# Optimization experiments

Measured on AMD Instinct MI355X. Metric: run time of the kernel, lower is better.

## Reference

```python
import jax, jax.numpy as jnp
import numpy as np

# Architecture constants pinned by the source script
D_MODEL = 2      # input_size / problemDim
ED = 64          # d_inner = expand_factor * d_model = hidden_size
N = 32           # d_state
K = 16           # d_conv
DT_RANK = 1      # ceil(d_model / 16)
NC = 4           # num_classes
B, L = 16, 2048


def setup_inputs() -> dict:
    key = jax.random.key(0)
    ks = jax.random.split(key, 16)
    rn = lambda k, shape, sc=0.1: jax.random.normal(k, shape, jnp.float32) * sc
    return {
        "x": jax.random.normal(ks[0], (B, L, D_MODEL), jnp.float32),
        "norm_w": jnp.ones((D_MODEL,), jnp.float32),
        "w_in": rn(ks[1], (D_MODEL, 2 * ED)),            # in_proj (no bias)
        "conv_w": rn(ks[2], (ED, 1, K)),                  # depthwise causal conv
        "conv_b": rn(ks[3], (ED,)),
        "w_xproj": rn(ks[4], (ED, DT_RANK + 2 * N)),      # x_proj (no bias)
        "w_dt": rn(ks[5], (DT_RANK, ED)),                 # dt_proj
        "b_dt": rn(ks[6], (ED,)),
        "A_log": jnp.log(jnp.tile(jnp.arange(1, N + 1, dtype=jnp.float32), (ED, 1))),
        "D_skip": jnp.ones((ED,), jnp.float32),
        "w_out": rn(ks[7], (ED, ED)),                     # out_proj (classifier mode: d_inner->d_inner)
        "b_out": rn(ks[8], (ED,)),
        "w_fc": rn(ks[9], (ED, ED)),
        "b_fc": rn(ks[10], (ED,)),
        "w_cls": rn(ks[11], (ED, NC)),
        "b_cls": rn(ks[12], (NC,)),
        "w_reg": rn(ks[13], (ED, 1)),
        "b_reg": rn(ks[14], (1,)),
    }


def _rmsnorm(x, w, eps=1e-5):
    return x * jax.lax.rsqrt(jnp.mean(x * x, axis=-1, keepdims=True) + eps) * w


def _silu(x):
    return x * jax.nn.sigmoid(x)


def reference(x, norm_w, w_in, conv_w, conv_b, w_xproj, w_dt, b_dt, A_log, D_skip,
              w_out, b_out, w_fc, b_fc, w_cls, b_cls, w_reg, b_reg):
    # --- Mamba block (n_layers = 1, classifier mode: no residual back to d_model) ---
    h = _rmsnorm(x, norm_w)                                # [B,L,D]
    xz = h @ w_in                                          # [B,L,2*ED]
    xb, z = jnp.split(xz, 2, axis=-1)
    # depthwise causal conv over time (torch pads K-1 both sides then slices [:L] == left-pad K-1)
    xc = jnp.transpose(xb, (0, 2, 1))                      # [B,ED,L]
    xc = jax.lax.conv_general_dilated(
        xc, conv_w, window_strides=(1,), padding=[(K - 1, 0)],
        feature_group_count=ED, dimension_numbers=("NCH", "OIH", "NCH"))
    xc = xc + conv_b[None, :, None]
    xb = _silu(jnp.transpose(xc, (0, 2, 1)))               # [B,L,ED]
    # input-dependent SSM parameters
    dbc = xb @ w_xproj                                     # [B,L,dt_rank+2N]
    delta = jax.nn.softplus(dbc[..., :DT_RANK] @ w_dt + b_dt)   # [B,L,ED]
    Bm = dbc[..., DT_RANK:DT_RANK + N]                     # [B,L,N]
    C = dbc[..., DT_RANK + N:]                             # [B,L,N]
    A = -jnp.exp(A_log)                                    # [ED,N]
    dA = jnp.exp(delta[..., None] * A)                     # [B,L,ED,N]
    dBx = delta[..., None] * Bm[:, :, None, :] * xb[..., None]  # [B,L,ED,N]

    # selective scan: h_t = dA_t * h_{t-1} + dBx_t ; y_t = <h_t, C_t>
    def step(hst, inp):
        dA_t, dBx_t, C_t = inp
        hst = dA_t * hst + dBx_t                           # [B,ED,N]
        y = jnp.einsum("ben,bn->be", hst, C_t)
        return hst, y

    h0 = jnp.zeros((x.shape[0], ED, N), x.dtype)
    xs = (jnp.transpose(dA, (1, 0, 2, 3)),
          jnp.transpose(dBx, (1, 0, 2, 3)),
          jnp.transpose(C, (1, 0, 2)))
    _, ys = jax.lax.scan(step, h0, xs)                     # [L,B,ED]
    y = jnp.transpose(ys, (1, 0, 2)) + D_skip * xb         # [B,L,ED]
    y = y * _silu(z)                                       # gate
    out = y @ w_out + b_out                                # [B,L,ED]

    last = out[:, -1, :]                                   # [B,ED]
    hs = jax.nn.relu(last @ w_fc + b_fc)
    class_logits = hs @ w_cls + b_cls                      # [B,NC]
    mass_pred = (hs @ w_reg + b_reg)[:, 0]                 # [B]
    return class_logits, mass_pred
```

## Files before the change

kernel.cpp:

```cpp
#include <hip/hip_runtime.h>
#include <math.h>

#define BB 16
#define LL 2048
#define ED 64
#define NN 32
#define KK 16
#define NCHUNK 64
#define CH 32
#define NBLK (BB * NCHUNK)
#define NSEG 4
#define CPS (NCHUNK / NSEG)
#define XS (ED + 4)

__global__ __launch_bounds__(256) void k1_featscan(
    const float* __restrict__ x, const float* __restrict__ norm_w,
    const float* __restrict__ w_in, const float* __restrict__ conv_w,
    const float* __restrict__ conv_b, const float* __restrict__ w_xproj,
    const float* __restrict__ w_dt, const float* __restrict__ b_dt,
    float* __restrict__ sbuf, float* __restrict__ dsumbuf,
    float* __restrict__ xlast, float* __restrict__ zl, float* __restrict__ cl)
{
    const int bx = blockIdx.x;
    const int b = bx >> 6, ti = bx & 63;
    const int l0 = ti * CH;
    const int tid = threadIdx.x;

    __shared__ __align__(16) float xbl[CH][XS];
    __shared__ float hh[2 * (CH + KK - 1)];
    __shared__ __align__(16) float wdt[ED];
    __shared__ __align__(16) float wxs[ED][NN];
    __shared__ float dsp[4][ED];
    __shared__ __align__(16) union U {
        float pre[CH + KK - 1][ED];
        struct {
            float2 dlrl[CH][ED];
            float bml[CH][36];
            float dtr[CH];
        } sb;
    } u;

    for (int idx = tid; idx < ED * NN; idx += 256) {
        int e = idx >> 5, j = idx & 31;
        wxs[e][j] = w_xproj[e * 65 + 1 + j];
    }
    if (tid < ED) wdt[tid] = w_xproj[tid * 65];

    if (tid < 2 * (CH + KK - 1)) {
        int p = tid >> 1, c = tid & 1;
        int l = l0 - (KK - 1) + p;
        hh[tid] = (l >= 0) ? x[(b * LL + l) * 2 + c] : 0.f;
    }
    __syncthreads();
    if (tid < CH + KK - 1) {
        float x0 = hh[2 * tid], x1 = hh[2 * tid + 1];
        float s = rsqrtf(0.5f * (x0 * x0 + x1 * x1) + 1e-5f);
        hh[2 * tid]     = x0 * s * norm_w[0];
        hh[2 * tid + 1] = x1 * s * norm_w[1];
    }
    __syncthreads();
    {
        const int e = tid & 63;
        const float w0 = w_in[e], w1 = w_in[128 + e];
        for (int idx = tid; idx < (CH + KK - 1) * ED; idx += 256) {
            int p = idx >> 6;
            u.pre[p][e] = hh[2 * p] * w0 + hh[2 * p + 1] * w1;
        }
    }
    __syncthreads();
    {
        const int e = tid & 63, tg = tid >> 6, t0 = tg * 8;
        const float4 c0 = *(const float4*)(conv_w + e * KK);
        const float4 c1 = *(const float4*)(conv_w + e * KK + 4);
        const float4 c2 = *(const float4*)(conv_w + e * KK + 8);
        const float4 c3 = *(const float4*)(conv_w + e * KK + 12);
        const float cw[KK] = {c0.x, c0.y, c0.z, c0.w, c1.x, c1.y, c1.z, c1.w,
                              c2.x, c2.y, c2.z, c2.w, c3.x, c3.y, c3.z, c3.w};
        float w[8 + KK - 1];
        #pragma unroll
        for (int i = 0; i < 8 + KK - 1; ++i) w[i] = u.pre[t0 + i][e];
        const float bias = conv_b[e];
        #pragma unroll
        for (int i = 0; i < 8; ++i) {
            float acc = bias;
            #pragma unroll
            for (int k = 0; k < KK; ++k) acc = __fmaf_rn(cw[k], w[i + k], acc);
            xbl[t0 + i][e] = acc / (1.f + __expf(-acc));
        }
    }
    __syncthreads();
    {
        const int t = tid & 31, jg = tid >> 5;
        float a0 = 0.f, a1 = 0.f, a2 = 0.f, a3 = 0.f;
        for (int e = 0; e < ED; e += 4) {
            const float4 xv = *(const float4*)&xbl[t][e];
            const float4 w0 = *(const float4*)&wxs[e + 0][jg * 4];
            const float4 w1 = *(const float4*)&wxs[e + 1][jg * 4];
            const float4 w2 = *(const float4*)&wxs[e + 2][jg * 4];
            const float4 w3 = *(const float4*)&wxs[e + 3][jg * 4];
            a0 = __fmaf_rn(xv.x, w0.x, a0); a1 = __fmaf_rn(xv.x, w0.y, a1);
            a2 = __fmaf_rn(xv.x, w0.z, a2); a3 = __fmaf_rn(xv.x, w0.w, a3);
            a0 = __fmaf_rn(xv.y, w1.x, a0); a1 = __fmaf_rn(xv.y, w1.y, a1);
            a2 = __fmaf_rn(xv.y, w1.z, a2); a3 = __fmaf_rn(xv.y, w1.w, a3);
            a0 = __fmaf_rn(xv.z, w2.x, a0); a1 = __fmaf_rn(xv.z, w2.y, a1);
            a2 = __fmaf_rn(xv.z, w2.z, a2); a3 = __fmaf_rn(xv.z, w2.w, a3);
            a0 = __fmaf_rn(xv.w, w3.x, a0); a1 = __fmaf_rn(xv.w, w3.y, a1);
            a2 = __fmaf_rn(xv.w, w3.z, a2); a3 = __fmaf_rn(xv.w, w3.w, a3);
        }
        u.sb.bml[t][jg * 4 + 0] = a0;
        u.sb.bml[t][jg * 4 + 1] = a1;
        u.sb.bml[t][jg * 4 + 2] = a2;
        u.sb.bml[t][jg * 4 + 3] = a3;
    }
    if (tid < CH) {
        float acc = 0.f;
        for (int e = 0; e < ED; e += 4) {
            const float4 xv = *(const float4*)&xbl[tid][e];
            const float4 wv = *(const float4*)&wdt[e];
            acc = __fmaf_rn(xv.x, wv.x, acc);
            acc = __fmaf_rn(xv.y, wv.y, acc);
            acc = __fmaf_rn(xv.z, wv.z, acc);
            acc = __fmaf_rn(xv.w, wv.w, acc);
        }
        u.sb.dtr[tid] = acc;
    }
    if (ti == NCHUNK - 1) {
        if (tid < NN) {
            float acc = 0.f;
            for (int e = 0; e < ED; ++e)
                acc = __fmaf_rn(xbl[CH - 1][e], w_xproj[e * 65 + 33 + tid], acc);
            cl[b * NN + tid] = acc;
        } else if (tid >= 64 && tid < 128) {
            int e = tid - 64;
            int pl = 2 * (CH + KK - 2);
            zl[b * ED + e] = hh[pl] * w_in[64 + e] + hh[pl + 1] * w_in[192 + e];
        } else if (tid >= 128 && tid < 192) {
            int e = tid - 128;
            xlast[b * ED + e] = xbl[CH - 1][e];
        }
    }
    __syncthreads();
    {
        const int e = tid & 63, tg = tid >> 6;
        const float wde = w_dt[e], bde = b_dt[e];
        float dpart = 0.f;
        #pragma unroll
        for (int k = 0; k < 8; ++k) {
            int s = tg + 4 * k;
            float v = __fmaf_rn(u.sb.dtr[s], wde, bde);
            float d = (v > 15.f) ? v : __logf(1.f + __expf(v));
            dpart += d;
            u.sb.dlrl[s][e] = make_float2(__expf(-d), d * xbl[s][e]);
        }
        dsp[tg][e] = dpart;
    }
    __syncthreads();
    {
        const int e = tid & 63, ng = tid >> 6, n0 = ng * 8;
        float S[8];
        #pragma unroll
        for (int j = 0; j < 8; ++j) S[j] = 0.f;

        for (int s = 0; s < CH; ++s) {
            const float2 rd = u.sb.dlrl[s][e];
            const float r = rd.x, dx = rd.y;
            const float4 b0 = *(const float4*)&u.sb.bml[s][n0];
            const float4 b1 = *(const float4*)&u.sb.bml[s][n0 + 4];
            float r2 = r * r, r4 = r2 * r2, r8 = r4 * r4;
            float bb1 = (ng & 1) ? r8 : 1.f;
            float bb2 = (ng & 2) ? r8 * r8 : 1.f;
            float m = r * bb1 * bb2;
            S[0] = __fmaf_rn(m, S[0], dx * b0.x); m *= r;
            S[1] = __fmaf_rn(m, S[1], dx * b0.y); m *= r;
            S[2] = __fmaf_rn(m, S[2], dx * b0.z); m *= r;
            S[3] = __fmaf_rn(m, S[3], dx * b0.w); m *= r;
            S[4] = __fmaf_rn(m, S[4], dx * b1.x); m *= r;
            S[5] = __fmaf_rn(m, S[5], dx * b1.y); m *= r;
            S[6] = __fmaf_rn(m, S[6], dx * b1.z); m *= r;
            S[7] = __fmaf_rn(m, S[7], dx * b1.w);
        }

        const int gbase = (ti * BB + b) * (ED * NN) + e * NN + n0;
        *(float4*)&sbuf[gbase]     = make_float4(S[0], S[1], S[2], S[3]);
        *(float4*)&sbuf[gbase + 4] = make_float4(S[4], S[5], S[6], S[7]);
        if (tid < 64) {
            float Dsum = dsp[0][tid] + dsp[1][tid] + dsp[2][tid] + dsp[3][tid];
            dsumbuf[(ti * BB + b) * ED + tid] = Dsum;
        }
    }
}

__global__ __launch_bounds__(256) void k2_fold(
    const float* __restrict__ sbuf, const float* __restrict__ dsumbuf,
    const float* __restrict__ A_log, float* __restrict__ hfin)
{
    const int tid = threadIdx.x;
    const int sid = tid & 63, seg = tid >> 6;
    const int state = blockIdx.x * 64 + sid;
    const int b = state >> 11, r = state & 2047;
    const int e = r >> 5, n = r & 31;
    const float A = -__expf(A_log[e * NN + n]);

    float M = 1.f, S = 0.f;
    const int c0 = seg * CPS;
    #pragma unroll
    for (int k = 0; k < CPS; ++k) {
        const int c = c0 + k;
        float m = __expf(A * dsumbuf[(c * BB + b) * ED + e]);
        S = __fmaf_rn(m, S, sbuf[(c * BB + b) * (ED * NN) + r]);
        M *= m;
    }

    __shared__ float Ms[NSEG][64], Ss[NSEG][64];
    Ms[seg][sid] = M;
    Ss[seg][sid] = S;
    __syncthreads();
    if (seg == 0) {
        float h = S;
        #pragma unroll
        for (int k = 1; k < NSEG; ++k)
            h = __fmaf_rn(Ms[k][sid], h, Ss[k][sid]);
        hfin[state] = h;
    }
}

__global__ __launch_bounds__(256) void k3_tail(
    const float* __restrict__ hfin, const float* __restrict__ cl,
    const float* __restrict__ zl, const float* __restrict__ xlast,
    const float* __restrict__ D_skip, const float* __restrict__ w_out,
    const float* __restrict__ b_out, const float* __restrict__ w_fc,
    const float* __restrict__ b_fc, const float* __restrict__ w_cls,
    const float* __restrict__ b_cls, const float* __restrict__ w_reg,
    const float* __restrict__ b_reg, float* __restrict__ out)
{
    const int b = blockIdx.x, tid = threadIdx.x;
    const int e = tid & 63, ng = tid >> 6, n0 = ng * 8;

    __shared__ float part[4][ED];
    __shared__ float ylds[ED], olds[ED], hlds[ED];

    float acc;
    {
        const float4 h0 = *(const float4*)&hfin[b * (ED * NN) + e * NN + n0];
        const float4 h1 = *(const float4*)&hfin[b * (ED * NN) + e * NN + n0 + 4];
        const float4 q0 = *(const float4*)&cl[b * NN + n0];
        const float4 q1 = *(const float4*)&cl[b * NN + n0 + 4];
        acc = h0.x * q0.x + h0.y * q0.y + h0.z * q0.z + h0.w * q0.w
            + h1.x * q1.x + h1.y * q1.y + h1.z * q1.z + h1.w * q1.w;
    }
    part[ng][e] = acc;
    __syncthreads();

    if (tid < ED) {
        float y = part[0][tid] + part[1][tid] + part[2][tid] + part[3][tid];
        y = __fmaf_rn(D_skip[tid], xlast[b * ED + tid], y);
        float z = zl[b * ED + tid];
        y *= z / (1.f + __expf(-z));
        ylds[tid] = y;
    }
    __syncthreads();

    if (tid < ED) {
        float a2 = b_out[tid];
        #pragma unroll 8
        for (int ee = 0; ee < ED; ++ee)
            a2 = __fmaf_rn(ylds[ee], w_out[ee * ED + tid], a2);
        olds[tid] = a2;
    }
    __syncthreads();

    if (tid < ED) {
        float a3 = b_fc[tid];
        #pragma unroll 8
        for (int ee = 0; ee < ED; ++ee)
            a3 = __fmaf_rn(olds[ee], w_fc[ee * ED + tid], a3);
        hlds[tid] = fmaxf(a3, 0.f);
    }
    __syncthreads();

    if (tid < 4) {
        float a4 = b_cls[tid];
        for (int ee = 0; ee < ED; ++ee)
            a4 = __fmaf_rn(hlds[ee], w_cls[ee * 4 + tid], a4);
        out[b * 4 + tid] = a4;
    } else if (tid == 4) {
        float a5 = b_reg[0];
        for (int ee = 0; ee < ED; ++ee)
            a5 = __fmaf_rn(hlds[ee], w_reg[ee], a5);
        out[BB * 4 + b] = a5;
    }
}

extern "C" void kernel_launch(void* const* d_in, const int* in_sizes, int n_in,
                              void* d_out, int out_size, void* d_ws, size_t ws_size,
                              hipStream_t stream) {
    const float* x       = (const float*)d_in[0];
    const float* norm_w  = (const float*)d_in[1];
    const float* w_in    = (const float*)d_in[2];
    const float* conv_w  = (const float*)d_in[3];
    const float* conv_b  = (const float*)d_in[4];
    const float* w_xproj = (const float*)d_in[5];
    const float* w_dt    = (const float*)d_in[6];
    const float* b_dt    = (const float*)d_in[7];
    const float* A_log   = (const float*)d_in[8];
    const float* D_skip  = (const float*)d_in[9];
    const float* w_out   = (const float*)d_in[10];
    const float* b_out   = (const float*)d_in[11];
    const float* w_fc    = (const float*)d_in[12];
    const float* b_fc    = (const float*)d_in[13];
    const float* w_cls   = (const float*)d_in[14];
    const float* b_cls   = (const float*)d_in[15];
    const float* w_reg   = (const float*)d_in[16];
    const float* b_reg   = (const float*)d_in[17];
    float* out = (float*)d_out;

    float* ws      = (float*)d_ws;
    float* sbuf    = ws;
    float* dsumbuf = sbuf + NCHUNK * BB * ED * NN;
    float* hfin    = dsumbuf + NCHUNK * BB * ED;
    float* xlast   = hfin + BB * ED * NN;
    float* zl      = xlast + BB * ED;
    float* cl      = zl + BB * ED;

    k1_featscan<<<NBLK, 256, 0, stream>>>(x, norm_w, w_in, conv_w, conv_b,
                                          w_xproj, w_dt, b_dt,
                                          sbuf, dsumbuf, xlast, zl, cl);
    k2_fold<<<(BB * ED * NN * NSEG) / 256, 256, 0, stream>>>(sbuf, dsumbuf,
                                                             A_log, hfin);
    k3_tail<<<BB, 256, 0, stream>>>(hfin, cl, zl, xlast, D_skip,
                                    w_out, b_out, w_fc, b_fc,
                                    w_cls, b_cls, w_reg, b_reg, out);
}
```

Baseline: 116.5 us.

## Fuse fold and tail kernels via atomic counter; broadcast B via readlane

Merges the fold and tail kernels into one launch. The first 16 blocks spin on a global atomic counter until every fold block has written hfin, then run the output head, which removes one kernel launch and its boundary. In the chunk scan, B values for the 32 timesteps are loaded into registers once and broadcast with readlane instead of being re-read from shared memory each step. The spin-wait assumes the waiting blocks stay co-resident with the rest of the grid and adds global atomic traffic. The counter is reset inside the preceding kernel.

```diff
diff --git a/kernel.cpp b/kernel.cpp
--- a/kernel.cpp
+++ b/kernel.cpp
@@ -11,7 +11,12 @@
 #define NBLK (BB * NCHUNK)
 #define NSEG 4
 #define CPS (NCHUNK / NSEG)
+#define NBLK2 ((BB * ED * NN * NSEG) / 256)
 #define XS (ED + 4)
+
+__device__ __forceinline__ float rlane(float v, int l) {
+    return __uint_as_float(__builtin_amdgcn_readlane(__float_as_uint(v), l));
+}
 
 __global__ __launch_bounds__(256) void k1_featscan(
     const float* __restrict__ x, const float* __restrict__ norm_w,
@@ -19,12 +24,15 @@
     const float* __restrict__ conv_b, const float* __restrict__ w_xproj,
     const float* __restrict__ w_dt, const float* __restrict__ b_dt,
     float* __restrict__ sbuf, float* __restrict__ dsumbuf,
-    float* __restrict__ xlast, float* __restrict__ zl, float* __restrict__ cl)
+    float* __restrict__ xlast, float* __restrict__ zl, float* __restrict__ cl,
+    unsigned* __restrict__ counter)
 {
     const int bx = blockIdx.x;
     const int b = bx >> 6, ti = bx & 63;
     const int l0 = ti * CH;
     const int tid = threadIdx.x;
+
+    if (bx == 0 && tid == 0) *counter = 0u;
 
     __shared__ __align__(16) float xbl[CH][XS];
     __shared__ float hh[2 * (CH + KK - 1)];
@@ -157,6 +165,8 @@
     __syncthreads();
     {
         const int e = tid & 63, ng = tid >> 6, n0 = ng * 8;
+        const int s_l = e & 31, hf = e >> 5;
+        const float4 q = *(const float4*)&u.sb.bml[s_l][n0 + 4 * hf];
         float S[8];
         #pragma unroll
         for (int j = 0; j < 8; ++j) S[j] = 0.f;
@@ -164,20 +174,22 @@
         for (int s = 0; s < CH; ++s) {
             const float2 rd = u.sb.dlrl[s][e];
             const float r = rd.x, dx = rd.y;
-            const float4 b0 = *(const float4*)&u.sb.bml[s][n0];
-            const float4 b1 = *(const float4*)&u.sb.bml[s][n0 + 4];
+            const float b0x = rlane(q.x, s),      b0y = rlane(q.y, s);
+            const float b0z = rlane(q.z, s),      b0w = rlane(q.w, s);
+            const float b1x = rlane(q.x, s + 32), b1y = rlane(q.y, s + 32);
+            const float b1z = rlane(q.z, s + 32), b1w = rlane(q.w, s + 32);
             float r2 = r * r, r4 = r2 * r2, r8 = r4 * r4;
             float bb1 = (ng & 1) ? r8 : 1.f;
             float bb2 = (ng & 2) ? r8 * r8 : 1.f;
             float m = r * bb1 * bb2;
-            S[0] = __fmaf_rn(m, S[0], dx * b0.x); m *= r;
-            S[1] = __fmaf_rn(m, S[1], dx * b0.y); m *= r;
-            S[2] = __fmaf_rn(m, S[2], dx * b0.z); m *= r;
-            S[3] = __fmaf_rn(m, S[3], dx * b0.w); m *= r;
-            S[4] = __fmaf_rn(m, S[4], dx * b1.x); m *= r;
-            S[5] = __fmaf_rn(m, S[5], dx * b1.y); m *= r;
-            S[6] = __fmaf_rn(m, S[6], dx * b1.z); m *= r;
-            S[7] = __fmaf_rn(m, S[7], dx * b1.w);
+            S[0] = __fmaf_rn(m, S[0], dx * b0x); m *= r;
+            S[1] = __fmaf_rn(m, S[1], dx * b0y); m *= r;
+            S[2] = __fmaf_rn(m, S[2], dx * b0z); m *= r;
+            S[3] = __fmaf_rn(m, S[3], dx * b0w); m *= r;
+            S[4] = __fmaf_rn(m, S[4], dx * b1x); m *= r;
+            S[5] = __fmaf_rn(m, S[5], dx * b1y); m *= r;
+            S[6] = __fmaf_rn(m, S[6], dx * b1z); m *= r;
+            S[7] = __fmaf_rn(m, S[7], dx * b1w);
         }
 
         const int gbase = (ti * BB + b) * (ED * NN) + e * NN + n0;
@@ -190,14 +202,22 @@
     }
 }
 
-__global__ __launch_bounds__(256) void k2_fold(
+__global__ __launch_bounds__(256) void k2_fold_tail(
     const float* __restrict__ sbuf, const float* __restrict__ dsumbuf,
-    const float* __restrict__ A_log, float* __restrict__ hfin)
+    const float* __restrict__ A_log, float* __restrict__ hfin,
+    unsigned* __restrict__ counter,
+    const float* __restrict__ cl, const float* __restrict__ zl,
+    const float* __restrict__ xlast, const float* __restrict__ D_skip,
+    const float* __restrict__ w_out, const float* __restrict__ b_out,
+    const float* __restrict__ w_fc, const float* __restrict__ b_fc,
+    const float* __restrict__ w_cls, const float* __restrict__ b_cls,
+    const float* __restrict__ w_reg, const float* __restrict__ b_reg,
+    float* __restrict__ out)
 {
     const int tid = threadIdx.x;
     const int sid = tid & 63, seg = tid >> 6;
     const int state = blockIdx.x * 64 + sid;
-    const int b = state >> 11, r = state & 2047;
+    const int bb = state >> 11, r = state & 2047;
     const int e = r >> 5, n = r & 31;
     const float A = -__expf(A_log[e * NN + n]);
 
@@ -206,8 +226,8 @@
     #pragma unroll
     for (int k = 0; k < CPS; ++k) {
         const int c = c0 + k;
-        float m = __expf(A * dsumbuf[(c * BB + b) * ED + e]);
-        S = __fmaf_rn(m, S, sbuf[(c * BB + b) * (ED * NN) + r]);
+        float m = __expf(A * dsumbuf[(c * BB + bb) * ED + e]);
+        S = __fmaf_rn(m, S, sbuf[(c * BB + bb) * (ED * NN) + r]);
         M *= m;
     }
 
@@ -222,33 +242,35 @@
             h = __fmaf_rn(Ms[k][sid], h, Ss[k][sid]);
         hfin[state] = h;
     }
-}
-
-__global__ __launch_bounds__(256) void k3_tail(
-    const float* __restrict__ hfin, const float* __restrict__ cl,
-    const float* __restrict__ zl, const float* __restrict__ xlast,
-    const float* __restrict__ D_skip, const float* __restrict__ w_out,
-    const float* __restrict__ b_out, const float* __restrict__ w_fc,
-    const float* __restrict__ b_fc, const float* __restrict__ w_cls,
-    const float* __restrict__ b_cls, const float* __restrict__ w_reg,
-    const float* __restrict__ b_reg, float* __restrict__ out)
-{
-    const int b = blockIdx.x, tid = threadIdx.x;
-    const int e = tid & 63, ng = tid >> 6, n0 = ng * 8;
-
+    __syncthreads();
+    if (tid == 0) {
+        __threadfence();
+        atomicAdd(counter, 1u);
+    }
+
+    if (blockIdx.x >= BB) return;
+    const int b = blockIdx.x;
+
+    if (tid == 0)
+        while (atomicAdd(counter, 0u) < (unsigned)NBLK2) {  }
+    __syncthreads();
+    __threadfence();
+
+    const int ng = tid >> 6, n0 = ng * 8;
     __shared__ float part[4][ED];
     __shared__ float ylds[ED], olds[ED], hlds[ED];
 
     float acc;
     {
-        const float4 h0 = *(const float4*)&hfin[b * (ED * NN) + e * NN + n0];
-        const float4 h1 = *(const float4*)&hfin[b * (ED * NN) + e * NN + n0 + 4];
+        const int ee = tid & 63;
+        const float4 h0 = *(const float4*)&hfin[b * (ED * NN) + ee * NN + n0];
+        const float4 h1 = *(const float4*)&hfin[b * (ED * NN) + ee * NN + n0 + 4];
         const float4 q0 = *(const float4*)&cl[b * NN + n0];
         const float4 q1 = *(const float4*)&cl[b * NN + n0 + 4];
         acc = h0.x * q0.x + h0.y * q0.y + h0.z * q0.z + h0.w * q0.w
             + h1.x * q1.x + h1.y * q1.y + h1.z * q1.z + h1.w * q1.w;
-    }
-    part[ng][e] = acc;
+        part[ng][ee] = acc;
+    }
     __syncthreads();
 
     if (tid < ED) {
@@ -321,13 +343,14 @@
     float* xlast   = hfin + BB * ED * NN;
     float* zl      = xlast + BB * ED;
     float* cl      = zl + BB * ED;
+    unsigned* counter = (unsigned*)(cl + BB * NN);
 
     k1_featscan<<<NBLK, 256, 0, stream>>>(x, norm_w, w_in, conv_w, conv_b,
                                           w_xproj, w_dt, b_dt,
-                                          sbuf, dsumbuf, xlast, zl, cl);
-    k2_fold<<<(BB * ED * NN * NSEG) / 256, 256, 0, stream>>>(sbuf, dsumbuf,
-                                                             A_log, hfin);
-    k3_tail<<<BB, 256, 0, stream>>>(hfin, cl, zl, xlast, D_skip,
-                                    w_out, b_out, w_fc, b_fc,
-                                    w_cls, b_cls, w_reg, b_reg, out);
+                                          sbuf, dsumbuf, xlast, zl, cl,
+                                          counter);
+    k2_fold_tail<<<NBLK2, 256, 0, stream>>>(sbuf, dsumbuf, A_log, hfin,
+                                            counter, cl, zl, xlast, D_skip,
+                                            w_out, b_out, w_fc, b_fc,
+                                            w_cls, b_cls, w_reg, b_reg, out);
 }
```

After: 131.9 us. 13.3% more time.
